# Kernel optimization log

Hardware: AMD Instinct MI355X
Metric: run time of the kernel (lower is better)

## Reference

```python
import jax, jax.numpy as jnp
import numpy as np

H = 256   # input_size
P = 256   # state_size
BATCH, L = 8, 4096
DT_MIN, DT_MAX = 1e-3, 1e-1
LN_EPS = 1e-5


def _hippo_params():
    # HiPPO-N matrix (num_blocks=1), eigendecomposition in numpy (float64 then cast)
    idx = np.arange(P, dtype=np.float64)
    s = np.sqrt(idx + 0.5)
    A = -np.outer(s, s)
    A = np.tril(A) - np.triu(A, 1)
    np.fill_diagonal(A, -0.5)
    ev, V = np.linalg.eig(A)
    order = np.argsort(ev.real)
    ev, V = ev[order], V[:, order]
    return ev, V


def setup_inputs() -> dict:
    key = jax.random.key(0)
    k_u, = jax.random.split(key, 1)
    ev, V = _hippo_params()
    rng = np.random.default_rng(0)
    log_lambda_real = np.log(-np.clip(ev.real, None, -1e-4)).astype(np.float32)
    lambda_imag = ev.imag.astype(np.float32)
    V_inv = np.linalg.inv(V)
    B_init = rng.standard_normal((P, H)) / np.sqrt(P)
    B_tilde = V_inv @ B_init.astype(np.complex128)
    C_init = rng.standard_normal((H, P)) / np.sqrt(P)
    C_tilde = C_init.astype(np.complex128) @ V
    log_delta = (rng.random(P) * (np.log(DT_MAX) - np.log(DT_MIN)) + np.log(DT_MIN)).astype(np.float32)
    return {
        "u": jax.random.normal(k_u, (BATCH, L, H), dtype=jnp.float32),
        "log_lambda_real": jnp.asarray(log_lambda_real),
        "lambda_imag": jnp.asarray(lambda_imag),
        "B_tilde_real": jnp.asarray(B_tilde.real, dtype=jnp.float32),
        "B_tilde_imag": jnp.asarray(B_tilde.imag, dtype=jnp.float32),
        "C_tilde_real": jnp.asarray(C_tilde.real, dtype=jnp.float32),
        "C_tilde_imag": jnp.asarray(C_tilde.imag, dtype=jnp.float32),
        "log_delta": jnp.asarray(log_delta),
        "gamma": jnp.ones((H,), dtype=jnp.float32),
        "beta": jnp.zeros((H,), dtype=jnp.float32),
    }


def _layernorm(x, gamma, beta):
    mu = jnp.mean(x, axis=-1, keepdims=True)
    var = jnp.mean(jnp.square(x - mu), axis=-1, keepdims=True)
    return (x - mu) * jax.lax.rsqrt(var + LN_EPS) * gamma + beta


def _ssm(h, log_lambda_real, lambda_imag, B_tilde_real, B_tilde_imag,
         C_tilde_real, C_tilde_imag, log_delta):
    # Continuous-time diagonal SSM params
    lam = -jnp.exp(log_lambda_real) + 1j * lambda_imag            # (P,) complex
    B_tilde = B_tilde_real + 1j * B_tilde_imag                     # (P,H)
    C_tilde = C_tilde_real + 1j * C_tilde_imag                     # (H,P)
    delta = jnp.exp(log_delta)                                     # (P,)
    # ZOH discretization (eq. 6 of the S5 paper)
    lambda_bar = jnp.exp(lam * delta)                              # (P,)
    B_bar = ((lambda_bar - 1.0) / lam)[:, None] * B_tilde          # (P,H)
    # Bu_k = B_bar @ u_k  ->  (B,L,P) complex
    Bu = jnp.einsum('blh,ph->blp', h.astype(jnp.complex64), B_bar.astype(jnp.complex64))
    # Parallel associative scan for x_k = lambda_bar * x_{k-1} + Bu_k
    a = jnp.broadcast_to(lambda_bar.astype(jnp.complex64), Bu.shape)
    def combine(c1, c2):
        a1, b1 = c1
        a2, b2 = c2
        return a1 * a2, a2 * b1 + b2
    _, xs = jax.lax.associative_scan(combine, (a, Bu), axis=1)     # (B,L,P)
    # Project back to real output: y = Re(C_tilde @ x)
    y = jnp.einsum('blp,hp->blh', xs, C_tilde.astype(jnp.complex64)).real
    return y


def reference(u, log_lambda_real, lambda_imag, B_tilde_real, B_tilde_imag,
              C_tilde_real, C_tilde_imag, log_delta, gamma, beta):
    # S5Block: pre-LayerNorm -> S5 SSM -> GELU -> residual
    h = _layernorm(u, gamma, beta)
    y = _ssm(h, log_lambda_real, lambda_imag, B_tilde_real, B_tilde_imag,
             C_tilde_real, C_tilde_imag, log_delta)
    return u + jax.nn.gelu(y)
```

## Files before the change

### kernel.cpp

```cpp
#include <hip/hip_runtime.h>
#include <math.h>

#define HDIM 256
#define PDIM 256
#define BATCH 8
#define LSEQ 4096
#define MTOT (BATCH * LSEQ)
#define NCHUNK 128
#define CHLEN 32

typedef __attribute__((ext_vector_type(8))) short bf16x8;
typedef __attribute__((ext_vector_type(4))) float f32x4;

__device__ __forceinline__ unsigned short f2bf(float f) {
    union { float f; unsigned int u; } v; v.f = f;
    unsigned int r = v.u + 0x7FFFu + ((v.u >> 16) & 1u);
    return (unsigned short)(r >> 16);
}
__device__ __forceinline__ float bf2f(unsigned int lo16) {
    union { unsigned int u; float f; } v; v.u = lo16 << 16;
    return v.f;
}

__device__ __forceinline__ void gload_lds16(const void* g, void* l) {
    __builtin_amdgcn_global_load_lds(
        (const __attribute__((address_space(1))) void*)g,
        (__attribute__((address_space(3))) void*)l, 16, 0, 0);
}

__global__ void wpack_k(const float* __restrict__ llr, const float* __restrict__ lim,
                        const float* __restrict__ ldl,
                        const float* __restrict__ Br, const float* __restrict__ Bi,
                        const float* __restrict__ Cr, const float* __restrict__ Ci,
                        unsigned short* __restrict__ W1t, unsigned short* __restrict__ W2t,
                        float* __restrict__ par) {
    int h = threadIdx.x;
    if (blockIdx.x < PDIM) {
        int p = blockIdx.x;
        float er = expf(llr[p]);
        float im = lim[p];
        float d  = expf(ldl[p]);
        float zr = -er * d, zi = im * d;
        float ea = expf(zr);
        float sz, cz; sincosf(zi, &sz, &cz);
        float ar = ea * cz, ai = ea * sz;
        float dr = -er, di = im;
        float den = dr * dr + di * di;
        float nr = ar - 1.0f, ni = ai;
        float cr = (nr * dr + ni * di) / den;
        float ci = (ni * dr - nr * di) / den;
        float br = Br[p * HDIM + h], bi = Bi[p * HDIM + h];
        W1t[(2 * p) * HDIM + h]     = f2bf(cr * br - ci * bi);
        W1t[(2 * p + 1) * HDIM + h] = f2bf(cr * bi + ci * br);
    } else if (blockIdx.x < 2 * PDIM) {
        int p = blockIdx.x - PDIM;
        W2t[h * (2 * PDIM) + 2 * p]     = f2bf(Cr[h * PDIM + p]);
        W2t[h * (2 * PDIM) + 2 * p + 1] = f2bf(-Ci[h * PDIM + p]);
    } else {
        int p = h;
        float er = expf(llr[p]);
        float im = lim[p];
        float d  = expf(ldl[p]);
        float zr = -er * d, zi = im * d;
        float ea = expf(zr);
        float sz, cz; sincosf(zi, &sz, &cz);
        float ar = ea * cz, ai = ea * sz;
        float dr = -er, di = im;
        float den = dr * dr + di * di;
        float nr = ar - 1.0f, ni = ai;
        float cr = (nr * dr + ni * di) / den;
        float ci = (ni * dr - nr * di) / den;
        float eC = expf((float)CHLEN * zr);
        float sC, cC;
        sincosf((float)CHLEN * zi, &sC, &cC);
        par[2 * p]            = ar;
        par[2 * p + 1]        = ai;
        par[512 + 2 * p]      = cr;
        par[512 + 2 * p + 1]  = ci;
        par[1024 + 2 * p]     = eC * cC;
        par[1024 + 2 * p + 1] = eC * sC;
    }
}

__launch_bounds__(256, 2)
__global__ void ln_gemm1_k(const float* __restrict__ u, const unsigned short* __restrict__ W1t,
                           unsigned short* __restrict__ Bu,
                           const float* __restrict__ gamma, const float* __restrict__ beta) {
    __shared__ __align__(16) unsigned short As[128 * 256];
    __shared__ __align__(16) unsigned short Bs[2][128 * 32];
    const int t = threadIdx.x;
    const int lane = t & 63, w = t >> 6;

    const int nbn  = (int)gridDim.x;
    const int flat = (int)blockIdx.y * nbn + (int)blockIdx.x;
    const int nwg  = nbn * (int)gridDim.y;
    const int tile = (flat & 7) * (nwg >> 3) + (flat >> 3);
    const int bn = tile % nbn, bm = tile / nbn;

    const int srow   = 32 * w + (lane >> 2);
    const int schunk = (lane & 3) ^ ((lane >> 3) & 3);
    const unsigned short* gB = W1t + (size_t)(bn * 128 + srow) * HDIM + schunk * 8;
    const int bl0 = (32 * w) * 32;
    const int bl1 = (32 * w + 16) * 32;

    gload_lds16(gB,             &Bs[0][bl0]);
    gload_lds16(gB + 16 * HDIM, &Bs[0][bl1]);

    const float4 g4 = *(const float4*)(gamma + lane * 4);
    const float4 b4 = *(const float4*)(beta + lane * 4);
    #pragma unroll 4
    for (int i = 0; i < 32; i++) {
        const int row = i * 4 + w;
        const float4 v = *(const float4*)(u + (size_t)(bm * 128 + row) * HDIM + lane * 4);
        float s  = v.x + v.y + v.z + v.w;
        float sq = v.x * v.x + v.y * v.y + v.z * v.z + v.w * v.w;
        #pragma unroll
        for (int o = 1; o < 64; o <<= 1) { s += __shfl_xor(s, o); sq += __shfl_xor(sq, o); }
        const float mu = s * (1.0f / HDIM);
        const float rs = rsqrtf(sq * (1.0f / HDIM) - mu * mu + 1e-5f);
        ushort4 o4;
        o4.x = f2bf((v.x - mu) * rs * g4.x + b4.x);
        o4.y = f2bf((v.y - mu) * rs * g4.y + b4.y);
        o4.z = f2bf((v.z - mu) * rs * g4.z + b4.z);
        o4.w = f2bf((v.w - mu) * rs * g4.w + b4.w);
        const int idx = row * 256 + ((((lane >> 1) ^ (row & 7)) << 3) + (lane & 1) * 4);
        *(ushort4*)&As[idx] = o4;
    }

    const int wm = (w & 1) * 64, wn = (w >> 1) * 64;
    const int mrow = lane & 15;
    const int rsw  = (mrow >> 1) & 3;
    const int cch  = lane >> 4;
    const int fcol = (cch ^ rsw) * 8;

    f32x4 acc[4][4] = {};
    constexpr int NT = HDIM / 32;

    __syncthreads();

    #pragma unroll
    for (int tt = 0; tt < NT; ++tt) {
        const int cur = tt & 1;
        if (tt + 1 < NT) {
            const int k0 = (tt + 1) * 32;
            gload_lds16(gB + k0,             &Bs[cur ^ 1][bl0]);
            gload_lds16(gB + 16 * HDIM + k0, &Bs[cur ^ 1][bl1]);
        }
        const int cb = tt * 4;
        bf16x8 fa[4], fb[4];
        #pragma unroll
        for (int i = 0; i < 4; i++) {
            const int r = wm + i * 16 + mrow;
            fa[i] = *(const bf16x8*)&As[r * 256 + (((cb + cch) ^ (r & 7)) << 3)];
            fb[i] = *(const bf16x8*)&Bs[cur][(wn + i * 16 + mrow) * 32 + fcol];
        }
        #pragma unroll
        for (int i = 0; i < 4; i++)
            #pragma unroll
            for (int j = 0; j < 4; j++)
                acc[i][j] = __builtin_amdgcn_mfma_f32_16x16x32_bf16(fa[i], fb[j], acc[i][j], 0, 0, 0);
        __syncthreads();
    }

    const int r0 = (lane >> 4) * 4, c0 = lane & 15;
    #pragma unroll
    for (int i = 0; i < 4; i++) {
        #pragma unroll
        for (int r = 0; r < 4; r++) {
            const size_t rowoff = (size_t)(bm * 128 + wm + i * 16 + r0 + r) * 512;
            #pragma unroll
            for (int j = 0; j < 4; j++)
                Bu[rowoff + bn * 128 + wn + j * 16 + c0] = f2bf(acc[i][j][r]);
        }
    }
}

__global__ void scan_reduce_k(const unsigned short* __restrict__ Bu,
                              const float* __restrict__ par, float* __restrict__ last) {
    int t = threadIdx.x;
    int lane = t & 63, g = t >> 6;
    int c = blockIdx.x * 4 + g, b = blockIdx.y;
    int p0 = lane * 4;
    float4 a01 = *(const float4*)(par + 2 * p0);
    float4 a23 = *(const float4*)(par + 2 * p0 + 4);
    float ar[4] = {a01.x, a01.z, a23.x, a23.z};
    float ai[4] = {a01.y, a01.w, a23.y, a23.w};
    float xr[4] = {0.f, 0.f, 0.f, 0.f}, xi[4] = {0.f, 0.f, 0.f, 0.f};
    const uint4* q = (const uint4*)(Bu + ((size_t)b * LSEQ + (size_t)c * CHLEN) * 512) + lane;
    #pragma unroll 8
    for (int j = 0; j < CHLEN; j++) {
        uint4 v = q[(size_t)j * 64];
        unsigned int vv[4] = {v.x, v.y, v.z, v.w};
        #pragma unroll
        for (int k = 0; k < 4; k++) {
            float vr = bf2f(vv[k] & 0xFFFFu), vi = bf2f(vv[k] >> 16);
            float nr = fmaf(ar[k], xr[k], fmaf(-ai[k], xi[k], vr));
            float ni = fmaf(ar[k], xi[k], fmaf(ai[k], xr[k], vi));
            xr[k] = nr; xi[k] = ni;
        }
    }
    float* lp = last + ((size_t)b * NCHUNK + c) * 512 + 2 * p0;
    *(float4*)lp       = make_float4(xr[0], xi[0], xr[1], xi[1]);
    *(float4*)(lp + 4) = make_float4(xr[2], xi[2], xr[3], xi[3]);
}

__global__ void scan_carry_k(const float* __restrict__ last, float* __restrict__ prefix,
                             const float* __restrict__ par) {
    int p = threadIdx.x, b = blockIdx.x;
    float Ar = par[1024 + 2 * p], Ai = par[1024 + 2 * p + 1];
    float Pr = 0.0f, Pi = 0.0f;
    const float2* lp = (const float2*)(last + (size_t)b * NCHUNK * 512) + p;
    float2* pp = (float2*)(prefix + (size_t)b * NCHUNK * 512) + p;
    for (int c0 = 0; c0 < NCHUNK; c0 += 16) {
        float2 v[16];
        #pragma unroll
        for (int j = 0; j < 16; j++) v[j] = lp[(size_t)(c0 + j) * 256];
        #pragma unroll
        for (int j = 0; j < 16; j++) {
            pp[(size_t)(c0 + j) * 256] = make_float2(Pr, Pi);
            float nr = fmaf(Ar, Pr, fmaf(-Ai, Pi, v[j].x));
            float ni = fmaf(Ar, Pi, fmaf(Ai, Pr, v[j].y));
            Pr = nr; Pi = ni;
        }
    }
}

__launch_bounds__(256, 2)
__global__ void apply_gemm2_k(const unsigned short* __restrict__ Bu,
                              const float* __restrict__ par,
                              const float* __restrict__ prefix,
                              const unsigned short* __restrict__ W2t,
                              const float* __restrict__ u, float* __restrict__ out) {
    __shared__ __align__(16) unsigned short Xs[32 * 512];
    __shared__ __align__(16) unsigned short Bs[2][256 * 32];
    const int t = threadIdx.x;
    const int lane = t & 63, w = t >> 6;
    const int c = blockIdx.x, b = blockIdx.y;
    const size_t row0 = (size_t)b * LSEQ + (size_t)c * CHLEN;

    const int srow   = 64 * w + (lane >> 2);
    const int schunk = (lane & 3) ^ ((lane >> 3) & 3);
    const unsigned short* gB = W2t + (size_t)srow * 512 + schunk * 8;
    const int bl0 = (64 * w) * 32;

    #pragma unroll
    for (int m = 0; m < 4; m++)
        gload_lds16(gB + m * 16 * 512, &Bs[0][bl0 + m * 16 * 32]);

    {
        const int p = t;
        const unsigned int* q = (const unsigned int*)(Bu + row0 * 512) + p;
        unsigned int vv[32];
        #pragma unroll
        for (int j = 0; j < 32; j++) vv[j] = q[(size_t)j * 256];
        const float2 P = ((const float2*)(prefix + ((size_t)b * NCHUNK + c) * 512))[p];
        const float ar = par[2 * p], ai = par[2 * p + 1];
        float xr = P.x, xi = P.y;
        #pragma unroll
        for (int j = 0; j < 32; j++) {
            float vr = bf2f(vv[j] & 0xFFFFu), vi = bf2f(vv[j] >> 16);
            float nr = fmaf(ar, xr, fmaf(-ai, xi, vr));
            float ni = fmaf(ar, xi, fmaf(ai, xr, vi));
            xr = nr; xi = ni;
            unsigned int pk = (unsigned int)f2bf(xr) | ((unsigned int)f2bf(xi) << 16);
            *(unsigned int*)&Xs[j * 512 + ((((p >> 2) ^ (j & 7)) << 3) + (p & 3) * 2)] = pk;
        }
    }

    const int mrow = lane & 15;
    const int rsw  = (mrow >> 1) & 3;
    const int cch  = lane >> 4;
    const int fcol = (cch ^ rsw) * 8;

    f32x4 acc[2][4] = {};
    constexpr int NT = 16;

    __syncthreads();

    #pragma unroll
    for (int tt = 0; tt < NT; ++tt) {
        const int cur = tt & 1;
        if (tt + 1 < NT) {
            const int k0 = (tt + 1) * 32;
            #pragma unroll
            for (int m = 0; m < 4; m++)
                gload_lds16(gB + m * 16 * 512 + k0, &Bs[cur ^ 1][bl0 + m * 16 * 32]);
        }
        const int cb = tt * 4;
        bf16x8 fa[2], fb[4];
        #pragma unroll
        for (int i = 0; i < 2; i++) {
            const int r = i * 16 + mrow;
            fa[i] = *(const bf16x8*)&Xs[r * 512 + (((cb + cch) ^ (r & 7)) << 3)];
        }
        #pragma unroll
        for (int j = 0; j < 4; j++)
            fb[j] = *(const bf16x8*)&Bs[cur][(64 * w + j * 16 + mrow) * 32 + fcol];
        #pragma unroll
        for (int i = 0; i < 2; i++)
            #pragma unroll
            for (int j = 0; j < 4; j++)
                acc[i][j] = __builtin_amdgcn_mfma_f32_16x16x32_bf16(fa[i], fb[j], acc[i][j], 0, 0, 0);
        __syncthreads();
    }

    const int r0 = (lane >> 4) * 4, c0 = lane & 15;
    #pragma unroll
    for (int i = 0; i < 2; i++) {
        #pragma unroll
        for (int r = 0; r < 4; r++) {
            const size_t rowoff = (row0 + i * 16 + r0 + r) * HDIM;
            #pragma unroll
            for (int j = 0; j < 4; j++) {
                const int col = 64 * w + j * 16 + c0;
                float y = acc[i][j][r];
                float z = 0.7978845608f * fmaf(0.044715f * y * y, y, y);
                float e = __expf(2.0f * z);
                float th = 1.0f - 2.0f / (e + 1.0f);
                float g = 0.5f * y * (1.0f + th);
                out[rowoff + col] = u[rowoff + col] + g;
            }
        }
    }
}

extern "C" void kernel_launch(void* const* d_in, const int* in_sizes, int n_in,
                              void* d_out, int out_size, void* d_ws, size_t ws_size,
                              hipStream_t stream) {
    const float* u   = (const float*)d_in[0];
    const float* llr = (const float*)d_in[1];
    const float* lim = (const float*)d_in[2];
    const float* Br  = (const float*)d_in[3];
    const float* Bi  = (const float*)d_in[4];
    const float* Cr  = (const float*)d_in[5];
    const float* Ci  = (const float*)d_in[6];
    const float* ldl = (const float*)d_in[7];
    const float* gam = (const float*)d_in[8];
    const float* bet = (const float*)d_in[9];
    float* out = (float*)d_out;

    float* ws     = (float*)d_ws;
    float* par    = ws;
    float* last   = ws + 2048;
    float* prefix = last + (size_t)BATCH * NCHUNK * 512;
    unsigned short* W1t = (unsigned short*)(prefix + (size_t)BATCH * NCHUNK * 512);
    unsigned short* W2t = W1t + 512 * HDIM;
    unsigned short* Bu  = W2t + HDIM * 512;

    wpack_k<<<2 * PDIM + 1, HDIM, 0, stream>>>(llr, lim, ldl, Br, Bi, Cr, Ci, W1t, W2t, par);

    ln_gemm1_k<<<dim3(512 / 128, MTOT / 128), 256, 0, stream>>>(u, W1t, Bu, gam, bet);

    scan_reduce_k<<<dim3(NCHUNK / 4, BATCH), 256, 0, stream>>>(Bu, par, last);
    scan_carry_k<<<BATCH, PDIM, 0, stream>>>(last, prefix, par);

    apply_gemm2_k<<<dim3(NCHUNK, BATCH), 256, 0, stream>>>(Bu, par, prefix, W2t, u, out);
}
```

Measured before the change: 178.9 us.

## Split LayerNorm into its own kernel and read GEMM operands directly from global

```diff
diff --git a/kernel.cpp b/kernel.cpp
--- a/kernel.cpp
+++ b/kernel.cpp
@@ -20,12 +20,6 @@
 __device__ __forceinline__ float bf2f(unsigned int lo16) {
     union { unsigned int u; float f; } v; v.u = lo16 << 16;
     return v.f;
-}
-
-__device__ __forceinline__ void gload_lds16(const void* g, void* l) {
-    __builtin_amdgcn_global_load_lds(
-        (const __attribute__((address_space(1))) void*)g,
-        (__attribute__((address_space(3))) void*)l, 16, 0, 0);
 }
 
 __global__ void wpack_k(const float* __restrict__ llr, const float* __restrict__ lim,
@@ -82,84 +76,57 @@
     }
 }
 
-__launch_bounds__(256, 2)
-__global__ void ln_gemm1_k(const float* __restrict__ u, const unsigned short* __restrict__ W1t,
-                           unsigned short* __restrict__ Bu,
-                           const float* __restrict__ gamma, const float* __restrict__ beta) {
-    __shared__ __align__(16) unsigned short As[128 * 256];
-    __shared__ __align__(16) unsigned short Bs[2][128 * 32];
+__global__ void ln_k(const float* __restrict__ u, unsigned short* __restrict__ hbf,
+                     const float* __restrict__ gamma, const float* __restrict__ beta) {
+    __shared__ float gS[HDIM], bS[HDIM];
+    int t = threadIdx.x;
+    gS[t] = gamma[t]; bS[t] = beta[t];
+    int lane = t & 63, wv = t >> 6;
+    int row = blockIdx.x * 4 + wv;
+    float4 v = *(const float4*)(u + (size_t)row * HDIM + lane * 4);
+    float s  = v.x + v.y + v.z + v.w;
+    float sq = v.x * v.x + v.y * v.y + v.z * v.z + v.w * v.w;
+    #pragma unroll
+    for (int o = 1; o < 64; o <<= 1) { s += __shfl_xor(s, o); sq += __shfl_xor(sq, o); }
+    float mu = s * (1.0f / HDIM);
+    float rs = rsqrtf(sq * (1.0f / HDIM) - mu * mu + 1e-5f);
+    __syncthreads();
+    int c = lane * 4;
+    ushort4 o;
+    o.x = f2bf((v.x - mu) * rs * gS[c + 0] + bS[c + 0]);
+    o.y = f2bf((v.y - mu) * rs * gS[c + 1] + bS[c + 1]);
+    o.z = f2bf((v.z - mu) * rs * gS[c + 2] + bS[c + 2]);
+    o.w = f2bf((v.w - mu) * rs * gS[c + 3] + bS[c + 3]);
+    *(ushort4*)(hbf + (size_t)row * HDIM + c) = o;
+}
+
+__launch_bounds__(512, 4)
+__global__ void gemm1_k(const unsigned short* __restrict__ A,
+                        const unsigned short* __restrict__ W1t,
+                        unsigned short* __restrict__ Bu) {
     const int t = threadIdx.x;
     const int lane = t & 63, w = t >> 6;
-
-    const int nbn  = (int)gridDim.x;
-    const int flat = (int)blockIdx.y * nbn + (int)blockIdx.x;
-    const int nwg  = nbn * (int)gridDim.y;
-    const int tile = (flat & 7) * (nwg >> 3) + (flat >> 3);
-    const int bn = tile % nbn, bm = tile / nbn;
-
-    const int srow   = 32 * w + (lane >> 2);
-    const int schunk = (lane & 3) ^ ((lane >> 3) & 3);
-    const unsigned short* gB = W1t + (size_t)(bn * 128 + srow) * HDIM + schunk * 8;
-    const int bl0 = (32 * w) * 32;
-    const int bl1 = (32 * w + 16) * 32;
-
-    gload_lds16(gB,             &Bs[0][bl0]);
-    gload_lds16(gB + 16 * HDIM, &Bs[0][bl1]);
-
-    const float4 g4 = *(const float4*)(gamma + lane * 4);
-    const float4 b4 = *(const float4*)(beta + lane * 4);
-    #pragma unroll 4
-    for (int i = 0; i < 32; i++) {
-        const int row = i * 4 + w;
-        const float4 v = *(const float4*)(u + (size_t)(bm * 128 + row) * HDIM + lane * 4);
-        float s  = v.x + v.y + v.z + v.w;
-        float sq = v.x * v.x + v.y * v.y + v.z * v.z + v.w * v.w;
-        #pragma unroll
-        for (int o = 1; o < 64; o <<= 1) { s += __shfl_xor(s, o); sq += __shfl_xor(sq, o); }
-        const float mu = s * (1.0f / HDIM);
-        const float rs = rsqrtf(sq * (1.0f / HDIM) - mu * mu + 1e-5f);
-        ushort4 o4;
-        o4.x = f2bf((v.x - mu) * rs * g4.x + b4.x);
-        o4.y = f2bf((v.y - mu) * rs * g4.y + b4.y);
-        o4.z = f2bf((v.z - mu) * rs * g4.z + b4.z);
-        o4.w = f2bf((v.w - mu) * rs * g4.w + b4.w);
-        const int idx = row * 256 + ((((lane >> 1) ^ (row & 7)) << 3) + (lane & 1) * 4);
-        *(ushort4*)&As[idx] = o4;
-    }
-
-    const int wm = (w & 1) * 64, wn = (w >> 1) * 64;
-    const int mrow = lane & 15;
-    const int rsw  = (mrow >> 1) & 3;
-    const int cch  = lane >> 4;
-    const int fcol = (cch ^ rsw) * 8;
+    const int bm = blockIdx.x;
+    const int mrow = lane & 15, cch = lane >> 4;
+
+    const unsigned short* gA = A   + (size_t)(bm * 64 + mrow) * HDIM + cch * 8;
+    const unsigned short* gW = W1t + (size_t)(w * 64 + mrow) * HDIM + cch * 8;
 
     f32x4 acc[4][4] = {};
-    constexpr int NT = HDIM / 32;
-
-    __syncthreads();
-
-    #pragma unroll
-    for (int tt = 0; tt < NT; ++tt) {
-        const int cur = tt & 1;
-        if (tt + 1 < NT) {
-            const int k0 = (tt + 1) * 32;
-            gload_lds16(gB + k0,             &Bs[cur ^ 1][bl0]);
-            gload_lds16(gB + 16 * HDIM + k0, &Bs[cur ^ 1][bl1]);
-        }
-        const int cb = tt * 4;
+    #pragma unroll
+    for (int tt = 0; tt < HDIM / 32; tt++) {
         bf16x8 fa[4], fb[4];
         #pragma unroll
-        for (int i = 0; i < 4; i++) {
-            const int r = wm + i * 16 + mrow;
-            fa[i] = *(const bf16x8*)&As[r * 256 + (((cb + cch) ^ (r & 7)) << 3)];
-            fb[i] = *(const bf16x8*)&Bs[cur][(wn + i * 16 + mrow) * 32 + fcol];
-        }
+        for (int i = 0; i < 4; i++)
+            fa[i] = *(const bf16x8*)(gA + (size_t)i * 16 * HDIM + tt * 32);
+        #pragma unroll
+        for (int j = 0; j < 4; j++)
+            fb[j] = *(const bf16x8*)(gW + (size_t)j * 16 * HDIM + tt * 32);
         #pragma unroll
         for (int i = 0; i < 4; i++)
             #pragma unroll
             for (int j = 0; j < 4; j++)
                 acc[i][j] = __builtin_amdgcn_mfma_f32_16x16x32_bf16(fa[i], fb[j], acc[i][j], 0, 0, 0);
-        __syncthreads();
     }
 
     const int r0 = (lane >> 4) * 4, c0 = lane & 15;
@@ -167,10 +134,10 @@
     for (int i = 0; i < 4; i++) {
         #pragma unroll
         for (int r = 0; r < 4; r++) {
-            const size_t rowoff = (size_t)(bm * 128 + wm + i * 16 + r0 + r) * 512;
+            const size_t rowoff = (size_t)(bm * 64 + i * 16 + r0 + r) * 512;
             #pragma unroll
             for (int j = 0; j < 4; j++)
-                Bu[rowoff + bn * 128 + wn + j * 16 + c0] = f2bf(acc[i][j][r]);
+                Bu[rowoff + w * 64 + j * 16 + c0] = f2bf(acc[i][j][r]);
         }
     }
 }
@@ -225,27 +192,17 @@
     }
 }
 
-__launch_bounds__(256, 2)
+__launch_bounds__(256, 4)
 __global__ void apply_gemm2_k(const unsigned short* __restrict__ Bu,
                               const float* __restrict__ par,
                               const float* __restrict__ prefix,
                               const unsigned short* __restrict__ W2t,
                               const float* __restrict__ u, float* __restrict__ out) {
     __shared__ __align__(16) unsigned short Xs[32 * 512];
-    __shared__ __align__(16) unsigned short Bs[2][256 * 32];
     const int t = threadIdx.x;
     const int lane = t & 63, w = t >> 6;
     const int c = blockIdx.x, b = blockIdx.y;
     const size_t row0 = (size_t)b * LSEQ + (size_t)c * CHLEN;
-
-    const int srow   = 64 * w + (lane >> 2);
-    const int schunk = (lane & 3) ^ ((lane >> 3) & 3);
-    const unsigned short* gB = W2t + (size_t)srow * 512 + schunk * 8;
-    const int bl0 = (64 * w) * 32;
-
-    #pragma unroll
-    for (int m = 0; m < 4; m++)
-        gload_lds16(gB + m * 16 * 512, &Bs[0][bl0 + m * 16 * 32]);
 
     {
         const int p = t;
@@ -267,41 +224,28 @@
         }
     }
 
-    const int mrow = lane & 15;
-    const int rsw  = (mrow >> 1) & 3;
-    const int cch  = lane >> 4;
-    const int fcol = (cch ^ rsw) * 8;
+    const int mrow = lane & 15, cch = lane >> 4;
+    const unsigned short* gW = W2t + (size_t)(w * 64 + mrow) * 512 + cch * 8;
 
     f32x4 acc[2][4] = {};
-    constexpr int NT = 16;
-
     __syncthreads();
 
     #pragma unroll
-    for (int tt = 0; tt < NT; ++tt) {
-        const int cur = tt & 1;
-        if (tt + 1 < NT) {
-            const int k0 = (tt + 1) * 32;
-            #pragma unroll
-            for (int m = 0; m < 4; m++)
-                gload_lds16(gB + m * 16 * 512 + k0, &Bs[cur ^ 1][bl0 + m * 16 * 32]);
-        }
-        const int cb = tt * 4;
+    for (int tt = 0; tt < 16; tt++) {
         bf16x8 fa[2], fb[4];
         #pragma unroll
         for (int i = 0; i < 2; i++) {
             const int r = i * 16 + mrow;
-            fa[i] = *(const bf16x8*)&Xs[r * 512 + (((cb + cch) ^ (r & 7)) << 3)];
+            fa[i] = *(const bf16x8*)&Xs[r * 512 + (((tt * 4 + cch) ^ (r & 7)) << 3)];
         }
         #pragma unroll
         for (int j = 0; j < 4; j++)
-            fb[j] = *(const bf16x8*)&Bs[cur][(64 * w + j * 16 + mrow) * 32 + fcol];
+            fb[j] = *(const bf16x8*)(gW + (size_t)j * 16 * 512 + tt * 32);
         #pragma unroll
         for (int i = 0; i < 2; i++)
             #pragma unroll
             for (int j = 0; j < 4; j++)
                 acc[i][j] = __builtin_amdgcn_mfma_f32_16x16x32_bf16(fa[i], fb[j], acc[i][j], 0, 0, 0);
-        __syncthreads();
     }
 
     const int r0 = (lane >> 4) * 4, c0 = lane & 15;
@@ -312,7 +256,7 @@
             const size_t rowoff = (row0 + i * 16 + r0 + r) * HDIM;
             #pragma unroll
             for (int j = 0; j < 4; j++) {
-                const int col = 64 * w + j * 16 + c0;
+                const int col = w * 64 + j * 16 + c0;
                 float y = acc[i][j][r];
                 float z = 0.7978845608f * fmaf(0.044715f * y * y, y, y);
                 float e = __expf(2.0f * z);
@@ -345,11 +289,13 @@
     float* prefix = last + (size_t)BATCH * NCHUNK * 512;
     unsigned short* W1t = (unsigned short*)(prefix + (size_t)BATCH * NCHUNK * 512);
     unsigned short* W2t = W1t + 512 * HDIM;
-    unsigned short* Bu  = W2t + HDIM * 512;
-
+    unsigned short* hbf = W2t + HDIM * 512;
+    unsigned short* Bu  = hbf + (size_t)MTOT * HDIM;
+
+    ln_k<<<MTOT / 4, 256, 0, stream>>>(u, hbf, gam, bet);
     wpack_k<<<2 * PDIM + 1, HDIM, 0, stream>>>(llr, lim, ldl, Br, Bi, Cr, Ci, W1t, W2t, par);
 
-    ln_gemm1_k<<<dim3(512 / 128, MTOT / 128), 256, 0, stream>>>(u, W1t, Bu, gam, bet);
+    gemm1_k<<<MTOT / 64, 512, 0, stream>>>(hbf, W1t, Bu);
 
     scan_reduce_k<<<dim3(NCHUNK / 4, BATCH), 256, 0, stream>>>(Bu, par, last);
     scan_carry_k<<<BATCH, PDIM, 0, stream>>>(last, prefix, par);
```

Result: slower. 193.5 us (+8.2%).
